# Kernel tuning notes

Measured on AMD Instinct MI355X. Metric: run time of the kernel, lower is better.

Reference implementation:

```python
import jax, jax.numpy as jnp
import numpy as np

EPS = 1e-12

def _l2norm(v):
    # torch.nn.functional.normalize(p=2) with eps clamp
    return v / jnp.maximum(jnp.linalg.norm(v), EPS)

def _spectral_weight(W, U):
    # W: (out, in) flattened 1x1 conv weight; U: (1, out) power-iteration buffer.
    # One power iteration, all under stop_gradient (torch.no_grad in original).
    V = _l2norm(U @ W)            # (1, in)
    Unew = _l2norm(V @ W.T)       # (1, out)
    sigma = (Unew @ W @ V.T)[0, 0]
    return W / jax.lax.stop_gradient(sigma)

def _conv1x1(x, W, b):
    # x: (b,c,h,w), W: (o,c), b: (o,)
    return jnp.einsum('oc,bchw->bohw', W, x) + b[None, :, None, None]

def setup_inputs() -> dict:
    key = jax.random.key(0)
    ks = jax.random.split(key, 11)
    B, C, H, W = 4, 256, 64, 64
    Ck = C // 8
    return {
        'x':   jax.random.normal(ks[0], (B, C, H, W), jnp.float32),
        'f_w': jax.random.normal(ks[1], (Ck, C), jnp.float32) * 0.05,
        'f_b': jax.random.normal(ks[2], (Ck,), jnp.float32) * 0.05,
        'f_u': jax.random.uniform(ks[3], (1, Ck), jnp.float32),
        'g_w': jax.random.normal(ks[4], (Ck, C), jnp.float32) * 0.05,
        'g_b': jax.random.normal(ks[5], (Ck,), jnp.float32) * 0.05,
        'g_u': jax.random.uniform(ks[6], (1, Ck), jnp.float32),
        'h_w': jax.random.normal(ks[7], (C, C), jnp.float32) * 0.05,
        'h_b': jax.random.normal(ks[8], (C,), jnp.float32) * 0.05,
        'h_u': jax.random.uniform(ks[9], (1, C), jnp.float32),
        'gamma': jax.random.normal(ks[10], (1, 1), jnp.float32),
    }

def reference(x, f_w, f_b, f_u, g_w, g_b, g_u, h_w, h_b, h_u, gamma):
    b, c, h, w = x.shape
    hw = h * w
    key_ = _conv1x1(x, _spectral_weight(f_w, f_u), f_b).reshape(b, -1, hw).transpose(0, 2, 1)  # (b,hw,ck)
    query = _conv1x1(x, _spectral_weight(g_w, g_u), g_b).reshape(b, -1, hw)                    # (b,ck,hw)
    attn = jax.nn.softmax(jnp.einsum('bnd,bdm->bnm', key_, query), axis=-1)                    # (b,hw,hw)
    value = _conv1x1(x, _spectral_weight(h_w, h_u), h_b).reshape(b, -1, hw)                    # (b,c,hw)
    out = jnp.einsum('bnm,bcm->bnc', attn, value)                                              # (b,hw,c)
    # Faithful to original: raw view of (b,hw,c) contiguous buffer into (b,c,h,w)
    out = out.reshape(b, c, h, w)
    return gamma[0, 0] * out + x
```

## Files before the change

### kernel.cpp

```cpp
#include <hip/hip_runtime.h>


constexpr int kC   = 256;
constexpr int kHW  = 4096;
constexpr int kB   = 4;
constexpr int kCHW = kC * kHW;

typedef short bf16x8 __attribute__((ext_vector_type(8)));
typedef float f32x4  __attribute__((ext_vector_type(4)));
typedef unsigned short u16;

__device__ __forceinline__ u16 f2bf(float f) {
    union { float f; unsigned u; } v; v.f = f;
    unsigned u = v.u;
    return (u16)((u + 0x7fffu + ((u >> 16) & 1u)) >> 16);
}
__device__ __forceinline__ float bf2f(u16 h) {
    union { unsigned u; float f; } v; v.u = ((unsigned)h) << 16;
    return v.f;
}

__global__ __launch_bounds__(1024) void k_sigma(
    const float* __restrict__ fw, const float* __restrict__ fu,
    const float* __restrict__ gw, const float* __restrict__ gu,
    const float* __restrict__ hww, const float* __restrict__ hu,
    float* __restrict__ sig, u16* __restrict__ wh, u16* __restrict__ wl)
{
    const int which = blockIdx.x;
    const float* W = which == 0 ? fw : (which == 1 ? gw : hww);
    const float* U = which == 0 ? fu : (which == 1 ? gu : hu);
    const int O = (which == 2) ? 256 : 32;
    const int t = threadIdx.x;

    __shared__ float par[4][256];
    __shared__ float red[256];
    __shared__ __align__(16) float Vv[256];

    {
        const int i = t & 255, och = t >> 8;
        int olim = O - och * 64; olim = olim < 0 ? 0 : (olim > 64 ? 64 : olim);
        float p = 0.f;
        for (int oo = 0; oo < olim; ++oo) {
            const int o = och * 64 + oo;
            p += U[o] * W[o * 256 + i];
        }
        par[och][i] = p;
    }
    __syncthreads();
    float t1 = 0.f;
    if (t < 256) {
        t1 = par[0][t] + par[1][t] + par[2][t] + par[3][t];
        red[t] = t1 * t1;
    }
    __syncthreads();
    for (int s = 128; s > 0; s >>= 1) { if (t < s) red[t] += red[t + s]; __syncthreads(); }
    if (t < 256) Vv[t] = t1 / fmaxf(sqrtf(red[0]), 1e-12f);
    __syncthreads();

    {
        const int o = t & 255, ich = t >> 8;
        float q = 0.f;
        if (o < O) {
            const float4* Wr = (const float4*)(W + (size_t)o * 256 + ich * 64);
            const float4* Vr = (const float4*)(&Vv[ich * 64]);
#pragma unroll
            for (int j = 0; j < 16; ++j) {
                const float4 w = Wr[j]; const float4 v = Vr[j];
                q += w.x * v.x + w.y * v.y + w.z * v.z + w.w * v.w;
            }
        }
        par[ich][o] = q;
    }
    __syncthreads();
    if (t < 256) {
        const float t2 = par[0][t] + par[1][t] + par[2][t] + par[3][t];
        red[t] = t2 * t2;
    }
    __syncthreads();
    for (int s = 128; s > 0; s >>= 1) { if (t < s) red[t] += red[t + s]; __syncthreads(); }
    if (t == 0) {
        const float s2 = red[0];
        sig[which] = fmaxf(sqrtf(s2), 1e-12f) / s2;
    }

    const int nElem = O * 256;
    const int gbase = (which == 0) ? 0 : (which == 1 ? 32 : 64);
    for (int i = t; i < nElem; i += 1024) {
        const int o = i >> 8, ci = i & 255;
        const int g = gbase + o;
        const int idx = ((g >> 4) * 8 + (ci >> 5)) * 512 + (g & 15) * 32 + (ci & 31);
        const float f = W[i];
        const u16 h = f2bf(f);
        wh[idx] = h;
        wl[idx] = f2bf(f - bf2f(h));
    }
}

__global__ __launch_bounds__(512) void k_proj(
    const float* __restrict__ x,
    const u16* __restrict__ wh, const u16* __restrict__ wl,
    const float* __restrict__ fb, const float* __restrict__ gb,
    const float* __restrict__ hb, const float* __restrict__ sig,
    u16* __restrict__ Kc, u16* __restrict__ Qc, u16* __restrict__ Vb)
{
    __shared__ __align__(16) float xs[256][64];
    __shared__ float bLDS[320];

    const int t = threadIdx.x;
    const int wave = t >> 6, lane = t & 63;
    const int quad = lane >> 4, l15 = lane & 15;
    const int b = blockIdx.y;
    const int n0 = blockIdx.x * 64;
    const int nch = wave & 3, cohalf = wave >> 2;

    {
        const int r4i = lane >> 4, c16 = lane & 15;
        const float* xg = x + (size_t)b * kCHW + (size_t)r4i * kHW + n0 + c16 * 4;
#pragma unroll
        for (int j = 0; j < 8; ++j) {
            const int cibase = (wave * 8 + j) * 4;
            __builtin_amdgcn_global_load_lds(
                (const __attribute__((address_space(1))) void*)(xg + (size_t)cibase * kHW),
                (__attribute__((address_space(3))) void*)&xs[cibase][0], 16, 0, 0);
        }
    }
    if (t < 320) bLDS[t] = (t < 32) ? fb[t] : (t < 64) ? gb[t - 32] : hb[t - 64];
    __syncthreads();

    const int n = nch * 16 + l15;
    bf16x8 bh[8], bl[8];
#pragma unroll
    for (int s = 0; s < 8; ++s) {
        union { u16 a[8]; bf16x8 v; } H, L;
#pragma unroll
        for (int j = 0; j < 8; ++j) {
            const float v = xs[s * 32 + quad * 8 + j][n];
            const u16 h = f2bf(v);
            H.a[j] = h; L.a[j] = f2bf(v - bf2f(h));
        }
        bh[s] = H.v; bl[s] = L.v;
    }

    const u16* whp = wh + l15 * 32 + quad * 8;
    const u16* wlp = wl + l15 * 32 + quad * 8;

    f32x4 acc[10] = {};
#pragma unroll
    for (int c = 0; c < 10; ++c) {
        const size_t base = (size_t)(cohalf * 10 + c) * 4096;
#pragma unroll
        for (int s = 0; s < 8; ++s) {
            const bf16x8 ah = *(const bf16x8*)(whp + base + s * 512);
            const bf16x8 al = *(const bf16x8*)(wlp + base + s * 512);
            acc[c] = __builtin_amdgcn_mfma_f32_16x16x32_bf16(ah, bh[s], acc[c], 0, 0, 0);
            acc[c] = __builtin_amdgcn_mfma_f32_16x16x32_bf16(ah, bl[s], acc[c], 0, 0, 0);
            acc[c] = __builtin_amdgcn_mfma_f32_16x16x32_bf16(al, bh[s], acc[c], 0, 0, 0);
        }
    }

    const float s0 = sig[0], s1 = sig[1], s2 = sig[2];
#pragma unroll
    for (int c = 0; c < 10; ++c) {
        const int cog0 = (cohalf * 10 + c) * 16;
        const float inv = (cog0 < 32) ? s0 : (cog0 < 64) ? s1 : s2;
#pragma unroll
        for (int r = 0; r < 4; ++r) {
            const int co = cog0 + quad * 4 + r;
            const float v = acc[c][r] * inv + bLDS[co];
            if (co < 64) {
                u16* H = (co < 32) ? Kc : Qc;
                const int d = co & 31;
                const u16 h = f2bf(v);
                const u16 l = f2bf(v - bf2f(h));
                const size_t off = (size_t)(b * kHW + n0 + n) * 64;
                H[off + d] = h;
                H[off + 32 + d] = l;
            } else {
                Vb[((size_t)b * kC + (co - 64)) * kHW + n0 + n] = f2bf(v);
            }
        }
    }
}

__global__ __launch_bounds__(512, 4) void k_attn(
    const u16* __restrict__ Kc, const u16* __restrict__ Qc,
    const u16* __restrict__ Vb,
    u16* __restrict__ Op, float2* __restrict__ St)
{
    __shared__ __align__(16) u16 Qt[2][4096];
    __shared__ __align__(16) u16 Pt[4096];
    __shared__ float2 stLDS[8][16];
    __shared__ float aLDS[64];

    const int t = threadIdx.x;
    const int wave = t >> 6, lane = t & 63;
    const int quad = lane >> 4, l15 = lane & 15;
    const int sg = wave >> 1, half = wave & 1;

    const int id = blockIdx.x;
    const int xcd = id & 7;
    const int b = xcd >> 1;
    const int nb0 = ((xcd & 1) * 32 + ((id >> 3) & 31)) * 64;
    const int mh = id >> 8;
    const int mt0 = mh * 16, mt1 = mt0 + 16;

    const u16* Kb  = Kc + (size_t)b * kHW * 64;
    const u16* Qb  = Qc + (size_t)b * kHW * 64;
    const u16* Vbb = Vb + (size_t)b * kC * kHW;

    const size_t krow = (size_t)(nb0 + sg * 16 + l15) * 64 + (size_t)quad * 8;
    const bf16x8 kh = *(const bf16x8*)(Kb + krow);
    const bf16x8 kl = *(const bf16x8*)(Kb + krow + 32);

    const u16* vrow[2];
#pragma unroll
    for (int ct = 0; ct < 2; ++ct)
        vrow[ct] = Vbb + (size_t)(wave * 32 + ct * 16 + l15) * kHW + quad * 8;

    const int qs_row = lane >> 3, qs_ch = lane & 7;

    f32x4 O[8] = {};
    float mrow = -1e30f, lrow = 0.f;
    bf16x8 vc[4], vn[4];

    {
        const int rloc = wave * 8 + qs_row;
        __builtin_amdgcn_global_load_lds(
            (const __attribute__((address_space(1))) void*)
                (Qb + (size_t)(mt0 * 64 + rloc) * 64 + ((qs_ch ^ (rloc & 7)) << 3)),
            (__attribute__((address_space(3))) void*)&Qt[0][wave * 512], 16, 0, 0);
    }
#pragma unroll
    for (int ct = 0; ct < 2; ++ct)
#pragma unroll
        for (int ks = 0; ks < 2; ++ks)
            vc[ct * 2 + ks] = *(const bf16x8*)(vrow[ct] + mt0 * 64 + ks * 32);

    for (int mt = mt0; mt < mt1; ++mt) {
        const int cur = mt & 1;
        const int m0 = mt * 64;

        __syncthreads();

        if (mt < mt1 - 1) {
            const int m0n = m0 + 64;
            const int rloc = wave * 8 + qs_row;
            __builtin_amdgcn_global_load_lds(
                (const __attribute__((address_space(1))) void*)
                    (Qb + (size_t)(m0n + rloc) * 64 + ((qs_ch ^ (rloc & 7)) << 3)),
                (__attribute__((address_space(3))) void*)&Qt[cur ^ 1][wave * 512], 16, 0, 0);
        }
        const int m0v = (mt < mt1 - 1) ? m0 + 64 : m0;
#pragma unroll
        for (int ct = 0; ct < 2; ++ct)
#pragma unroll
            for (int ks = 0; ks < 2; ++ks)
                vn[ct * 2 + ks] = *(const bf16x8*)(vrow[ct] + m0v + ks * 32);

        f32x4 s[2];
#pragma unroll
        for (int mi2 = 0; mi2 < 2; ++mi2) {
            const int mi = half * 2 + mi2;
            const int rbase = (mi * 16 + l15) * 64;
            const bf16x8 qhv = *(const bf16x8*)&Qt[cur][rbase + ((quad       ^ (l15 & 7)) << 3)];
            const bf16x8 qlv = *(const bf16x8*)&Qt[cur][rbase + (((quad + 4) ^ (l15 & 7)) << 3)];
            f32x4 a = { 0.f, 0.f, 0.f, 0.f };
            a = __builtin_amdgcn_mfma_f32_16x16x32_bf16(qhv, kl, a, 0, 0, 0);
            a = __builtin_amdgcn_mfma_f32_16x16x32_bf16(qlv, kh, a, 0, 0, 0);
            a = __builtin_amdgcn_mfma_f32_16x16x32_bf16(qhv, kh, a, 0, 0, 0);
            s[mi2] = a;
        }

        float lm = s[0][0];
#pragma unroll
        for (int mi2 = 0; mi2 < 2; ++mi2)
#pragma unroll
            for (int r = 0; r < 4; ++r) lm = fmaxf(lm, s[mi2][r]);
        lm = fmaxf(lm, __shfl_xor(lm, 16));
        lm = fmaxf(lm, __shfl_xor(lm, 32));
        float ls = 0.f;
#pragma unroll
        for (int mi2 = 0; mi2 < 2; ++mi2)
#pragma unroll
            for (int r = 0; r < 4; ++r) {
                const float p = __expf(s[mi2][r] - lm);
                s[mi2][r] = p;
                ls += p;
            }
        ls += __shfl_xor(ls, 16);
        ls += __shfl_xor(ls, 32);
        if (lane < 16) stLDS[wave][l15] = make_float2(lm, ls);

        asm volatile("s_waitcnt lgkmcnt(0)\n\ts_barrier" ::: "memory");

        const float2 o2 = stLDS[wave ^ 1][l15];
        const float mnew = fmaxf(mrow, fmaxf(lm, o2.x));
        const float alpha = __expf(mrow - mnew);
        const float bm = __expf(lm - mnew);
        lrow = lrow * alpha + ls * bm + o2.y * __expf(o2.x - mnew);
        mrow = mnew;

        {
            const int prow = sg * 16 + l15;
#pragma unroll
            for (int mi2 = 0; mi2 < 2; ++mi2) {
                const float p0 = s[mi2][0] * bm, p1 = s[mi2][1] * bm;
                const float p2 = s[mi2][2] * bm, p3 = s[mi2][3] * bm;
                const unsigned d0 = __builtin_amdgcn_perm(
                    __float_as_uint(p1), __float_as_uint(p0), 0x07060302u);
                const unsigned d1 = __builtin_amdgcn_perm(
                    __float_as_uint(p3), __float_as_uint(p2), 0x07060302u);
                const int mi = half * 2 + mi2;
                const int chunk = 2 * mi + (quad >> 1);
                const int off = prow * 64 + ((chunk ^ (l15 & 7)) << 3) + (quad & 1) * 4;
                *(uint2*)(Pt + off) = make_uint2(d0, d1);
            }
            if (half == 0 && lane < 16) aLDS[sg * 16 + l15] = alpha;
        }

        asm volatile("s_waitcnt lgkmcnt(0)\n\ts_barrier" ::: "memory");

#pragma unroll
        for (int rg = 0; rg < 4; ++rg) {
            const float4 af = *(const float4*)&aLDS[rg * 16 + quad * 4];
#pragma unroll
            for (int ct = 0; ct < 2; ++ct) {
                O[rg * 2 + ct][0] *= af.x;
                O[rg * 2 + ct][1] *= af.y;
                O[rg * 2 + ct][2] *= af.z;
                O[rg * 2 + ct][3] *= af.w;
            }
        }

#pragma unroll
        for (int ks = 0; ks < 2; ++ks) {
#pragma unroll
            for (int rg = 0; rg < 4; ++rg) {
                const bf16x8 pa = *(const bf16x8*)&Pt[(rg * 16 + l15) * 64
                                     + (((ks * 4 + quad) ^ (l15 & 7)) << 3)];
#pragma unroll
                for (int ct = 0; ct < 2; ++ct)
                    O[rg * 2 + ct] = __builtin_amdgcn_mfma_f32_16x16x32_bf16(
                        pa, vc[ct * 2 + ks], O[rg * 2 + ct], 0, 0, 0);
            }
        }

#pragma unroll
        for (int i = 0; i < 4; ++i) vc[i] = vn[i];
    }

    if (half == 0 && lane < 16)
        St[(size_t)(mh * 4 + b) * kHW + nb0 + sg * 16 + l15] = make_float2(mrow, lrow);

    u16* Opb = Op + (size_t)(mh * 4 + b) * kHW * 256;
#pragma unroll
    for (int rg = 0; rg < 4; ++rg) {
#pragma unroll
        for (int ct = 0; ct < 2; ++ct) {
#pragma unroll
            for (int r = 0; r < 4; ++r) {
                const int nn = nb0 + rg * 16 + quad * 4 + r;
                const int c = wave * 32 + ct * 16 + l15;
                Opb[(size_t)nn * 256 + c] = f2bf(O[rg * 2 + ct][r]);
            }
        }
    }
}

__global__ __launch_bounds__(256) void k_merge(
    const float* __restrict__ x, const float* __restrict__ gamma,
    const u16* __restrict__ Op, const float2* __restrict__ St,
    float* __restrict__ out)
{
    const int tid = blockIdx.x * 256 + threadIdx.x;
    const int cg = tid & 31;
    const int n  = (tid >> 5) & 4095;
    const int b  = tid >> 17;
    const int c0 = cg * 8;

    float2 st[4];
#pragma unroll
    for (int q = 0; q < 4; ++q) st[q] = St[(size_t)(q * 4 + b) * kHW + n];
    float M = st[0].x;
#pragma unroll
    for (int q = 1; q < 4; ++q) M = fmaxf(M, st[q].x);
    float w[4], L = 0.f;
#pragma unroll
    for (int q = 0; q < 4; ++q) { w[q] = __expf(st[q].x - M); L += st[q].y * w[q]; }
    const float invL = 1.f / L;
#pragma unroll
    for (int q = 0; q < 4; ++q) w[q] *= invL;
    const float g = gamma[0];

    const size_t base = ((size_t)b * kHW + n) * 256 + c0;
    uint4 A[4];
#pragma unroll
    for (int q = 0; q < 4; ++q)
        A[q] = *(const uint4*)(Op + base + (size_t)q * 4 * kHW * 256);
    const float4 x0 = *(const float4*)(x + base);
    const float4 x1 = *(const float4*)(x + base + 4);

    float o[8];
#pragma unroll
    for (int j = 0; j < 8; ++j) {
        float acc = 0.f;
#pragma unroll
        for (int q = 0; q < 4; ++q) {
            const unsigned word = (j >> 1) == 0 ? A[q].x : (j >> 1) == 1 ? A[q].y
                                 : (j >> 1) == 2 ? A[q].z : A[q].w;
            acc += bf2f((u16)(word >> ((j & 1) * 16))) * w[q];
        }
        o[j] = acc;
    }
    float4 r0, r1;
    r0.x = g * o[0] + x0.x; r0.y = g * o[1] + x0.y;
    r0.z = g * o[2] + x0.z; r0.w = g * o[3] + x0.w;
    r1.x = g * o[4] + x1.x; r1.y = g * o[5] + x1.y;
    r1.z = g * o[6] + x1.z; r1.w = g * o[7] + x1.w;
    *(float4*)(out + base)     = r0;
    *(float4*)(out + base + 4) = r1;
}

extern "C" void kernel_launch(void* const* d_in, const int* in_sizes, int n_in,
                              void* d_out, int out_size, void* d_ws, size_t ws_size,
                              hipStream_t stream)
{
    const float* x     = (const float*)d_in[0];
    const float* fw    = (const float*)d_in[1];
    const float* fb    = (const float*)d_in[2];
    const float* fu    = (const float*)d_in[3];
    const float* gw    = (const float*)d_in[4];
    const float* gb    = (const float*)d_in[5];
    const float* gu    = (const float*)d_in[6];
    const float* hww   = (const float*)d_in[7];
    const float* hb    = (const float*)d_in[8];
    const float* hu    = (const float*)d_in[9];
    const float* gamma = (const float*)d_in[10];
    float* out = (float*)d_out;

    char* ws = (char*)d_ws;
    float* sig = (float*)ws;
    u16* wh = (u16*)(ws + 1024);
    u16* wl = wh + 320 * 256;
    u16* Kc = (u16*)(ws + (1u << 20));
    u16* Qc = (u16*)(ws + (3u << 20));
    u16* Vb = (u16*)(ws + (5u << 20));
    u16* Op = (u16*)(ws + (16u << 20));
    float2* St = (float2*)(ws + (48u << 20));

    k_sigma<<<dim3(3), dim3(1024), 0, stream>>>(fw, fu, gw, gu, hww, hu, sig, wh, wl);
    k_proj<<<dim3(64, 4), dim3(512), 0, stream>>>(x, wh, wl, fb, gb, hb, sig,
                                                  Kc, Qc, Vb);
    k_attn<<<dim3(1024), dim3(512), 0, stream>>>(Kc, Qc, Vb, Op, St);
    k_merge<<<dim3(2048), dim3(256), 0, stream>>>(x, gamma, Op, St, out);
}
```

Measured before the change: 260.8 us.

## Restructure attention kernel into 256-thread blocks with per-wave softmax state

The attention kernel now runs 256-thread blocks covering 32 query rows. Each pair of waves handles one half of every 64-column key tile and keeps its own running max and sum, so the cross-wave max/sum exchange and one barrier per iteration go away. The partials still form four sets for the merge kernel. Q and V fragments are read straight from global memory instead of being staged through LDS with a prefetch, so load latency is no longer hidden. Smaller row tiles also halve V reuse per block, which raises L2 traffic. A minor unroll pragma is added to the power-iteration loop.

Measured after the change: 344.8 us. 32.2% more time.

```diff
diff --git a/kernel.cpp b/kernel.cpp
--- a/kernel.cpp
+++ b/kernel.cpp
@@ -40,6 +40,7 @@
         const int i = t & 255, och = t >> 8;
         int olim = O - och * 64; olim = olim < 0 ? 0 : (olim > 64 ? 64 : olim);
         float p = 0.f;
+#pragma unroll 8
         for (int oo = 0; oo < olim; ++oo) {
             const int o = och * 64 + oo;
             p += U[o] * W[o * 256 + i];
@@ -182,27 +183,26 @@
     }
 }
 
-__global__ __launch_bounds__(512, 4) void k_attn(
+__global__ __launch_bounds__(256, 4) void k_attn(
     const u16* __restrict__ Kc, const u16* __restrict__ Qc,
     const u16* __restrict__ Vb,
     u16* __restrict__ Op, float2* __restrict__ St)
 {
-    __shared__ __align__(16) u16 Qt[2][4096];
-    __shared__ __align__(16) u16 Pt[4096];
-    __shared__ float2 stLDS[8][16];
-    __shared__ float aLDS[64];
+    __shared__ __align__(16) u16 Pb[2][2][32][40];
+    __shared__ float aB[2][2][32];
 
     const int t = threadIdx.x;
     const int wave = t >> 6, lane = t & 63;
     const int quad = lane >> 4, l15 = lane & 15;
-    const int sg = wave >> 1, half = wave & 1;
+    const int sg = wave & 1, h = wave >> 1;
 
     const int id = blockIdx.x;
     const int xcd = id & 7;
     const int b = xcd >> 1;
-    const int nb0 = ((xcd & 1) * 32 + ((id >> 3) & 31)) * 64;
-    const int mh = id >> 8;
-    const int mt0 = mh * 16, mt1 = mt0 + 16;
+    const int slot = (xcd & 1) * 128 + (id >> 3);
+    const int rb = slot & 127, mh = slot >> 7;
+    const int nb0 = rb * 32;
+    const int mt0 = mh * 32, mt1 = mt0 + 32;
 
     const u16* Kb  = Kc + (size_t)b * kHW * 64;
     const u16* Qb  = Qc + (size_t)b * kHW * 64;
@@ -212,62 +212,28 @@
     const bf16x8 kh = *(const bf16x8*)(Kb + krow);
     const bf16x8 kl = *(const bf16x8*)(Kb + krow + 32);
 
-    const u16* vrow[2];
-#pragma unroll
-    for (int ct = 0; ct < 2; ++ct)
-        vrow[ct] = Vbb + (size_t)(wave * 32 + ct * 16 + l15) * kHW + quad * 8;
-
-    const int qs_row = lane >> 3, qs_ch = lane & 7;
-
-    f32x4 O[8] = {};
+    f32x4 O[16] = {};
     float mrow = -1e30f, lrow = 0.f;
-    bf16x8 vc[4], vn[4];
-
-    {
-        const int rloc = wave * 8 + qs_row;
-        __builtin_amdgcn_global_load_lds(
-            (const __attribute__((address_space(1))) void*)
-                (Qb + (size_t)(mt0 * 64 + rloc) * 64 + ((qs_ch ^ (rloc & 7)) << 3)),
-            (__attribute__((address_space(3))) void*)&Qt[0][wave * 512], 16, 0, 0);
-    }
-#pragma unroll
-    for (int ct = 0; ct < 2; ++ct)
-#pragma unroll
-        for (int ks = 0; ks < 2; ++ks)
-            vc[ct * 2 + ks] = *(const bf16x8*)(vrow[ct] + mt0 * 64 + ks * 32);
 
     for (int mt = mt0; mt < mt1; ++mt) {
         const int cur = mt & 1;
         const int m0 = mt * 64;
 
-        __syncthreads();
-
-        if (mt < mt1 - 1) {
-            const int m0n = m0 + 64;
-            const int rloc = wave * 8 + qs_row;
-            __builtin_amdgcn_global_load_lds(
-                (const __attribute__((address_space(1))) void*)
-                    (Qb + (size_t)(m0n + rloc) * 64 + ((qs_ch ^ (rloc & 7)) << 3)),
-                (__attribute__((address_space(3))) void*)&Qt[cur ^ 1][wave * 512], 16, 0, 0);
-        }
-        const int m0v = (mt < mt1 - 1) ? m0 + 64 : m0;
-#pragma unroll
-        for (int ct = 0; ct < 2; ++ct)
-#pragma unroll
-            for (int ks = 0; ks < 2; ++ks)
-                vn[ct * 2 + ks] = *(const bf16x8*)(vrow[ct] + m0v + ks * 32);
+        bf16x8 qh[2], ql[2];
+#pragma unroll
+        for (int mi2 = 0; mi2 < 2; ++mi2) {
+            const size_t qoff = (size_t)(m0 + h * 32 + mi2 * 16 + l15) * 64 + quad * 8;
+            qh[mi2] = *(const bf16x8*)(Qb + qoff);
+            ql[mi2] = *(const bf16x8*)(Qb + qoff + 32);
+        }
 
         f32x4 s[2];
 #pragma unroll
         for (int mi2 = 0; mi2 < 2; ++mi2) {
-            const int mi = half * 2 + mi2;
-            const int rbase = (mi * 16 + l15) * 64;
-            const bf16x8 qhv = *(const bf16x8*)&Qt[cur][rbase + ((quad       ^ (l15 & 7)) << 3)];
-            const bf16x8 qlv = *(const bf16x8*)&Qt[cur][rbase + (((quad + 4) ^ (l15 & 7)) << 3)];
             f32x4 a = { 0.f, 0.f, 0.f, 0.f };
-            a = __builtin_amdgcn_mfma_f32_16x16x32_bf16(qhv, kl, a, 0, 0, 0);
-            a = __builtin_amdgcn_mfma_f32_16x16x32_bf16(qlv, kh, a, 0, 0, 0);
-            a = __builtin_amdgcn_mfma_f32_16x16x32_bf16(qhv, kh, a, 0, 0, 0);
+            a = __builtin_amdgcn_mfma_f32_16x16x32_bf16(qh[mi2], kl, a, 0, 0, 0);
+            a = __builtin_amdgcn_mfma_f32_16x16x32_bf16(ql[mi2], kh, a, 0, 0, 0);
+            a = __builtin_amdgcn_mfma_f32_16x16x32_bf16(qh[mi2], kh, a, 0, 0, 0);
             s[mi2] = a;
         }
 
@@ -278,90 +244,77 @@
             for (int r = 0; r < 4; ++r) lm = fmaxf(lm, s[mi2][r]);
         lm = fmaxf(lm, __shfl_xor(lm, 16));
         lm = fmaxf(lm, __shfl_xor(lm, 32));
+        const float mnew = fmaxf(mrow, lm);
+        const float alpha = __expf(mrow - mnew);
         float ls = 0.f;
 #pragma unroll
         for (int mi2 = 0; mi2 < 2; ++mi2)
 #pragma unroll
             for (int r = 0; r < 4; ++r) {
-                const float p = __expf(s[mi2][r] - lm);
+                const float p = __expf(s[mi2][r] - mnew);
                 s[mi2][r] = p;
                 ls += p;
             }
         ls += __shfl_xor(ls, 16);
         ls += __shfl_xor(ls, 32);
-        if (lane < 16) stLDS[wave][l15] = make_float2(lm, ls);
+        lrow = lrow * alpha + ls;
+        mrow = mnew;
+
+        {
+            u16* Pw = &Pb[cur][h][sg * 16 + l15][0];
+#pragma unroll
+            for (int mi2 = 0; mi2 < 2; ++mi2) {
+                const unsigned d0 = __builtin_amdgcn_perm(
+                    __float_as_uint(s[mi2][1]), __float_as_uint(s[mi2][0]), 0x07060302u);
+                const unsigned d1 = __builtin_amdgcn_perm(
+                    __float_as_uint(s[mi2][3]), __float_as_uint(s[mi2][2]), 0x07060302u);
+                *(uint2*)(Pw + mi2 * 16 + quad * 4) = make_uint2(d0, d1);
+            }
+            if (lane < 16) aB[cur][h][sg * 16 + l15] = alpha;
+        }
 
         asm volatile("s_waitcnt lgkmcnt(0)\n\ts_barrier" ::: "memory");
 
-        const float2 o2 = stLDS[wave ^ 1][l15];
-        const float mnew = fmaxf(mrow, fmaxf(lm, o2.x));
-        const float alpha = __expf(mrow - mnew);
-        const float bm = __expf(lm - mnew);
-        lrow = lrow * alpha + ls * bm + o2.y * __expf(o2.x - mnew);
-        mrow = mnew;
-
-        {
-            const int prow = sg * 16 + l15;
-#pragma unroll
-            for (int mi2 = 0; mi2 < 2; ++mi2) {
-                const float p0 = s[mi2][0] * bm, p1 = s[mi2][1] * bm;
-                const float p2 = s[mi2][2] * bm, p3 = s[mi2][3] * bm;
-                const unsigned d0 = __builtin_amdgcn_perm(
-                    __float_as_uint(p1), __float_as_uint(p0), 0x07060302u);
-                const unsigned d1 = __builtin_amdgcn_perm(
-                    __float_as_uint(p3), __float_as_uint(p2), 0x07060302u);
-                const int mi = half * 2 + mi2;
-                const int chunk = 2 * mi + (quad >> 1);
-                const int off = prow * 64 + ((chunk ^ (l15 & 7)) << 3) + (quad & 1) * 4;
-                *(uint2*)(Pt + off) = make_uint2(d0, d1);
-            }
-            if (half == 0 && lane < 16) aLDS[sg * 16 + l15] = alpha;
-        }
-
-        asm volatile("s_waitcnt lgkmcnt(0)\n\ts_barrier" ::: "memory");
-
-#pragma unroll
-        for (int rg = 0; rg < 4; ++rg) {
-            const float4 af = *(const float4*)&aLDS[rg * 16 + quad * 4];
-#pragma unroll
-            for (int ct = 0; ct < 2; ++ct) {
-                O[rg * 2 + ct][0] *= af.x;
-                O[rg * 2 + ct][1] *= af.y;
-                O[rg * 2 + ct][2] *= af.z;
-                O[rg * 2 + ct][3] *= af.w;
-            }
-        }
-
-#pragma unroll
-        for (int ks = 0; ks < 2; ++ks) {
-#pragma unroll
-            for (int rg = 0; rg < 4; ++rg) {
-                const bf16x8 pa = *(const bf16x8*)&Pt[(rg * 16 + l15) * 64
-                                     + (((ks * 4 + quad) ^ (l15 & 7)) << 3)];
-#pragma unroll
-                for (int ct = 0; ct < 2; ++ct)
-                    O[rg * 2 + ct] = __builtin_amdgcn_mfma_f32_16x16x32_bf16(
-                        pa, vc[ct * 2 + ks], O[rg * 2 + ct], 0, 0, 0);
-            }
-        }
-
-#pragma unroll
-        for (int i = 0; i < 4; ++i) vc[i] = vn[i];
-    }
-
-    if (half == 0 && lane < 16)
-        St[(size_t)(mh * 4 + b) * kHW + nb0 + sg * 16 + l15] = make_float2(mrow, lrow);
-
-    u16* Opb = Op + (size_t)(mh * 4 + b) * kHW * 256;
-#pragma unroll
-    for (int rg = 0; rg < 4; ++rg) {
-#pragma unroll
-        for (int ct = 0; ct < 2; ++ct) {
+#pragma unroll
+        for (int rt = 0; rt < 2; ++rt) {
+            const float4 af = *(const float4*)&aB[cur][h][rt * 16 + quad * 4];
+#pragma unroll
+            for (int ct = 0; ct < 8; ++ct) {
+                O[rt * 8 + ct][0] *= af.x;
+                O[rt * 8 + ct][1] *= af.y;
+                O[rt * 8 + ct][2] *= af.z;
+                O[rt * 8 + ct][3] *= af.w;
+            }
+        }
+
+        const int vmb = m0 + h * 32 + quad * 8;
+#pragma unroll
+        for (int rt = 0; rt < 2; ++rt) {
+            const bf16x8 pa = *(const bf16x8*)&Pb[cur][h][rt * 16 + l15][quad * 8];
+#pragma unroll
+            for (int ct = 0; ct < 8; ++ct) {
+                const bf16x8 vb8 = *(const bf16x8*)(
+                    Vbb + (size_t)(sg * 128 + ct * 16 + l15) * kHW + vmb);
+                O[rt * 8 + ct] = __builtin_amdgcn_mfma_f32_16x16x32_bf16(
+                    pa, vb8, O[rt * 8 + ct], 0, 0, 0);
+            }
+        }
+    }
+
+    const int set = mh * 2 + h;
+    if (lane < 16)
+        St[(size_t)(set * 4 + b) * kHW + nb0 + sg * 16 + l15] = make_float2(mrow, lrow);
+
+    u16* Opb = Op + (size_t)(set * 4 + b) * kHW * 256;
+#pragma unroll
+    for (int rt = 0; rt < 2; ++rt) {
+#pragma unroll
+        for (int ct = 0; ct < 8; ++ct) {
 #pragma unroll
             for (int r = 0; r < 4; ++r) {
-                const int nn = nb0 + rg * 16 + quad * 4 + r;
-                const int c = wave * 32 + ct * 16 + l15;
-                Opb[(size_t)nn * 256 + c] = f2bf(O[rg * 2 + ct][r]);
+                const int nn = nb0 + rt * 16 + quad * 4 + r;
+                const int c = sg * 128 + ct * 16 + l15;
+                Opb[(size_t)nn * 256 + c] = f2bf(O[rt * 8 + ct][r]);
             }
         }
     }
@@ -451,6 +404,6 @@
     k_sigma<<<dim3(3), dim3(1024), 0, stream>>>(fw, fu, gw, gu, hww, hu, sig, wh, wl);
     k_proj<<<dim3(64, 4), dim3(512), 0, stream>>>(x, wh, wl, fb, gb, hb, sig,
                                                   Kc, Qc, Vb);
-    k_attn<<<dim3(1024), dim3(512), 0, stream>>>(Kc, Qc, Vb, Op, St);
+    k_attn<<<dim3(1024), dim3(256), 0, stream>>>(Kc, Qc, Vb, Op, St);
     k_merge<<<dim3(2048), dim3(256), 0, stream>>>(x, gamma, Op, St, out);
 }
```
